# Kernel optimization log

Hardware: AMD Instinct MI355X
Metric: run time of the kernel (lower is better)

## Reference

```python
import jax, jax.numpy as jnp
import numpy as np

R, E, A, F, K = 1024, 512, 128, 32, 31  # rnn_dim, embed_dim, attn_dim, n_filters, kernel
B, T = 64, 2048


def setup_inputs() -> dict:
    key = jax.random.key(0)
    ks = jax.random.split(key, 10)
    return {
        "attention_hidden": jax.random.normal(ks[0], (B, R), jnp.float32),
        "memory": jax.random.normal(ks[1], (B, T, E), jnp.float32),
        "attention_weights_cat": jax.random.uniform(ks[2], (B, 2, T), jnp.float32),
        "mask": jax.random.randint(ks[3], (B, T), 0, 2, jnp.int32),
        "W_query": jax.random.normal(ks[4], (R, A), jnp.float32) / np.sqrt(R),
        "W_memory": jax.random.normal(ks[5], (E, A), jnp.float32) / np.sqrt(E),
        "conv_w": jax.random.normal(ks[6], (F, 2, K), jnp.float32) / np.sqrt(2 * K),  # OIH
        "W_loc": jax.random.normal(ks[7], (F, A), jnp.float32) / np.sqrt(F),
        "v_w": jax.random.normal(ks[8], (A,), jnp.float32) / np.sqrt(A),
        "v_b": jax.random.normal(ks[9], (1,), jnp.float32) * 0.0,
    }


def reference(attention_hidden, memory, attention_weights_cat, mask,
              W_query, W_memory, conv_w, W_loc, v_w, v_b):
    # processed query: (B, A)
    pq = attention_hidden @ W_query
    # processed memory: (B, T, A)
    pm = jnp.einsum('bte,ea->bta', memory, W_memory)
    # location features: conv1d over (B, 2, T) with 'same' padding, no bias
    loc = jax.lax.conv_general_dilated(
        attention_weights_cat, conv_w,
        window_strides=(1,), padding=[((K - 1) // 2, (K - 1) // 2)],
        dimension_numbers=('NCH', 'OIH', 'NCH'))  # (B, F, T)
    pl = jnp.einsum('bft,fa->bta', loc, W_loc)  # (B, T, A)
    # energies: v(tanh(pm + pq + pl)) -> (B, T)
    energies = jnp.tanh(pm + pq[:, None, :] + pl) @ v_w + v_b[0]
    alignments = energies + mask.astype(energies.dtype) * -1e25
    attention_weights = jax.nn.softmax(alignments, axis=-1)
    # NOTE: original code (faithfully) uses raw alignments, not softmax weights
    attention_output = jnp.einsum('bt,bte->be', alignments, memory)
    return attention_output, attention_weights
```

## Files before the change

kernel.cpp:

```cpp
#include <hip/hip_runtime.h>

#define Bsz 64
#define Tsz 2048
#define Esz 512
#define Asz 128
#define Rsz 1024
#define KP  576
#define TILE_M 32
#define CHUNKS (Tsz / TILE_M)

typedef __bf16 bf16;
typedef __bf16 bf16x8 __attribute__((ext_vector_type(8)));
typedef __bf16 bf16x4 __attribute__((ext_vector_type(4)));
typedef __bf16 bf16x2 __attribute__((ext_vector_type(2)));
typedef float  f32x4  __attribute__((ext_vector_type(4)));


__global__ __launch_bounds__(256) void prep_kernel(
    const float* __restrict__ Wmem, const float* __restrict__ convw,
    const float* __restrict__ Wloc, const float* __restrict__ ah,
    const float* __restrict__ Wq, bf16* __restrict__ Wext,
    float* __restrict__ pq)
{
  __shared__ f32x4 red[256];
  int blk = blockIdx.x, tid = threadIdx.x;
  if (blk < 128) {
    int a = blk;
    #pragma unroll
    for (int e = tid; e < Esz; e += 256)
      Wext[(size_t)(e >> 3)*(Asz*8) + a*8 + (e & 7)] = (bf16)Wmem[e*Asz + a];
  } else if (blk < 160) {
    int idx = (blk - 128)*256 + tid;
    int a = idx >> 6, j = idx & 63;
    float u = 0.f;
    if (j < 62) {
      int c  = (j < 31) ? 0 : 1;
      int kk = (j < 31) ? j : j - 31;
      #pragma unroll
      for (int f = 0; f < 32; ++f)
        u += convw[f*62 + c*31 + kk] * Wloc[f*Asz + a];
    }
    Wext[(size_t)(64 + (j >> 3))*(Asz*8) + a*8 + (j & 7)] = (bf16)u;
  } else {
    int b  = blk - 160;
    int cg = tid & 31;
    int kg = tid >> 5;
    const float* ahb = ah + (size_t)b*Rsz;
    f32x4 s = (f32x4){0.f,0.f,0.f,0.f};
    int r0 = kg*128;
    for (int r = r0; r < r0 + 128; ++r) {
      float av = ahb[r];
      f32x4 wq = *(const f32x4*)&Wq[r*Asz + cg*4];
      s += av * wq;
    }
    red[tid] = s;
    __syncthreads();
    if (tid < 32) {
      f32x4 tot = red[tid];
      #pragma unroll
      for (int g = 1; g < 8; ++g) tot += red[g*32 + tid];
      *(f32x4*)&pq[b*Asz + tid*4] = tot;
    }
  }
}

__device__ __forceinline__ float tanh_fast(float x) {
  float ex = __expf(2.f * x);
  return 1.f - 2.f / (ex + 1.f);
}

template<bool USE_POUT>
__global__ __launch_bounds__(256, 4) void attn_main(
    const float* __restrict__ memory, const float* __restrict__ awcat,
    const int* __restrict__ mask, const bf16* __restrict__ Wext,
    const float* __restrict__ pq, const float* __restrict__ vw,
    const float* __restrict__ vb, float* __restrict__ pout,
    float* __restrict__ outg, float* __restrict__ ws_align)
{
  __shared__ bf16  Afull[TILE_M * KP];
  __shared__ float s_pq[Asz];
  __shared__ float s_vw[Asz];
  __shared__ float s_ebuf[TILE_M];
  __shared__ float s_align[TILE_M];

  int tid = threadIdx.x;
  int b  = blockIdx.x >> 6;
  int t0 = (blockIdx.x & 63) << 5;

  int w = tid >> 6, l = tid & 63;
  int quad = l >> 4, lrow = l & 15;
  int acol0 = w*32 + lrow;
  int acol1 = acol0 + 16;
  const bf16x8* wv = (const bf16x8*)Wext;

  bf16x8 bnext0 = wv[quad*Asz + acol0];
  bf16x8 bnext1 = wv[quad*Asz + acol1];

  const f32x4* memv = (const f32x4*)(memory + (size_t)(b*Tsz + t0)*Esz);
  #pragma unroll
  for (int p = 0; p < 16; ++p) {
    int i = tid + p*256;
    int r = i >> 7, c4 = i & 127;
    f32x4 v = __builtin_nontemporal_load(memv + r*128 + c4);
    int k = c4 * 4;
    int sw = (k >> 3) ^ (r & 7);
    int base = r*KP + sw*8 + (k & 7);
    bf16x4 pk; pk[0]=(bf16)v[0]; pk[1]=(bf16)v[1]; pk[2]=(bf16)v[2]; pk[3]=(bf16)v[3];
    *(bf16x4*)&Afull[base] = pk;
  }
  const float* aw = awcat + (size_t)b*2*Tsz;
  #pragma unroll
  for (int p = 0; p < 8; ++p) {
    int i = tid + p*256;
    int r = i >> 6, j = i & 63;
    float val = 0.f;
    if (j < 62) {
      int c  = (j < 31) ? 0 : 1;
      int kk = (j < 31) ? j : j - 31;
      int t  = t0 + r + kk - 15;
      if (t >= 0 && t < Tsz) val = aw[c*Tsz + t];
    }
    int k = Esz + j;
    int sw = (k >> 3) ^ (r & 7);
    Afull[r*KP + sw*8 + (k & 7)] = (bf16)val;
  }
  if (tid < Asz) { s_pq[tid] = pq[b*Asz + tid]; s_vw[tid] = vw[tid]; }
  if (tid < TILE_M) s_ebuf[tid] = 0.f;
  __syncthreads();

  f32x4 acc[2][2];
  #pragma unroll
  for (int mt = 0; mt < 2; ++mt)
    #pragma unroll
    for (int nt = 0; nt < 2; ++nt)
      acc[mt][nt] = (f32x4){0.f, 0.f, 0.f, 0.f};

  for (int kc = 0; kc < KP/32; ++kc) {
    bf16x8 bfrag0 = bnext0, bfrag1 = bnext1;
    if (kc < KP/32 - 1) {
      int kg2 = (kc+1)*4 + quad;
      bnext0 = wv[kg2*Asz + acol0];
      bnext1 = wv[kg2*Asz + acol1];
    }
    int kg = kc*4 + quad;
    bf16x8 afrag[2];
    #pragma unroll
    for (int mt = 0; mt < 2; ++mt) {
      int row = mt*16 + lrow;
      afrag[mt] = *(const bf16x8*)&Afull[row*KP + ((kg ^ (row & 7)) << 3)];
    }
    #pragma unroll
    for (int mt = 0; mt < 2; ++mt) {
      acc[mt][0] = __builtin_amdgcn_mfma_f32_16x16x32_bf16(afrag[mt], bfrag0, acc[mt][0], 0, 0, 0);
      acc[mt][1] = __builtin_amdgcn_mfma_f32_16x16x32_bf16(afrag[mt], bfrag1, acc[mt][1], 0, 0, 0);
    }
  }

  float partial[2][4];
  #pragma unroll
  for (int mt = 0; mt < 2; ++mt)
    #pragma unroll
    for (int rg = 0; rg < 4; ++rg) partial[mt][rg] = 0.f;
  #pragma unroll
  for (int nt = 0; nt < 2; ++nt) {
    int col = w*32 + nt*16 + lrow;
    float vwc = s_vw[col], pqc = s_pq[col];
    #pragma unroll
    for (int mt = 0; mt < 2; ++mt)
      #pragma unroll
      for (int rg = 0; rg < 4; ++rg)
        partial[mt][rg] += tanh_fast(acc[mt][nt][rg] + pqc) * vwc;
  }
  #pragma unroll
  for (int off = 1; off < 16; off <<= 1)
    #pragma unroll
    for (int mt = 0; mt < 2; ++mt)
      #pragma unroll
      for (int rg = 0; rg < 4; ++rg)
        partial[mt][rg] += __shfl_xor(partial[mt][rg], off, 64);
  if (lrow == 0) {
    #pragma unroll
    for (int mt = 0; mt < 2; ++mt)
      #pragma unroll
      for (int rg = 0; rg < 4; ++rg)
        atomicAdd(&s_ebuf[mt*16 + quad*4 + rg], partial[mt][rg]);
  }
  __syncthreads();

  if (tid < TILE_M) {
    int t = t0 + tid;
    float al = s_ebuf[tid] + vb[0] + (float)mask[b*Tsz + t] * -1e25f;
    s_align[tid] = al;
    ws_align[b*Tsz + t] = al;
  }
  __syncthreads();

  int k0 = tid * 2;
  float a0 = 0.f, a1 = 0.f;
  #pragma unroll
  for (int r = 0; r < TILE_M; ++r) {
    float al = s_align[r];
    int sw = ((k0 >> 3) ^ (r & 7));
    bf16x2 m = *(const bf16x2*)&Afull[r*KP + sw*8 + (k0 & 7)];
    a0 += al * (float)m[0];
    a1 += al * (float)m[1];
  }
  if constexpr (USE_POUT) {
    float2 o; o.x = a0; o.y = a1;
    *(float2*)&pout[(size_t)blockIdx.x * Esz + k0] = o;
  } else {
    atomicAdd(&outg[b*Esz + k0],     a0);
    atomicAdd(&outg[b*Esz + k0 + 1], a1);
  }
}

template<bool REDUCE>
__global__ __launch_bounds__(256) void softmax_kernel(
    const float* __restrict__ ws_align, const float* __restrict__ pout,
    float* __restrict__ out_be, float* __restrict__ out_w)
{
  int b = blockIdx.x, tid = threadIdx.x;
  const float* row = ws_align + (size_t)b*Tsz;
  float vals[8];
  float lmax = -3.4e38f;
  #pragma unroll
  for (int i = 0; i < 8; ++i) { vals[i] = row[tid + i*256]; lmax = fmaxf(lmax, vals[i]); }
  #pragma unroll
  for (int off = 1; off < 64; off <<= 1) lmax = fmaxf(lmax, __shfl_xor(lmax, off, 64));
  __shared__ float smax[4], ssum[4];
  if ((tid & 63) == 0) smax[tid >> 6] = lmax;
  __syncthreads();
  float bmax = fmaxf(fmaxf(smax[0], smax[1]), fmaxf(smax[2], smax[3]));
  float lsum = 0.f;
  #pragma unroll
  for (int i = 0; i < 8; ++i) { vals[i] = __expf(vals[i] - bmax); lsum += vals[i]; }
  #pragma unroll
  for (int off = 1; off < 64; off <<= 1) lsum += __shfl_xor(lsum, off, 64);
  if ((tid & 63) == 0) ssum[tid >> 6] = lsum;
  __syncthreads();
  float inv = 1.f / (ssum[0] + ssum[1] + ssum[2] + ssum[3]);
  #pragma unroll
  for (int i = 0; i < 8; ++i) out_w[(size_t)b*Tsz + tid + i*256] = vals[i] * inv;

  if constexpr (REDUCE) {
    float2 s; s.x = 0.f; s.y = 0.f;
    const float2* pv = (const float2*)(pout + (size_t)b*CHUNKS*Esz) + tid;
    #pragma unroll
    for (int c = 0; c < CHUNKS; ++c) {
      float2 v = pv[(size_t)c * (Esz/2)];
      s.x += v.x; s.y += v.y;
    }
    *(float2*)&out_be[(size_t)b*Esz + tid*2] = s;
  }
}

extern "C" void kernel_launch(void* const* d_in, const int* in_sizes, int n_in,
                              void* d_out, int out_size, void* d_ws, size_t ws_size,
                              hipStream_t stream) {
  const float* ah   = (const float*)d_in[0];
  const float* mem  = (const float*)d_in[1];
  const float* awc  = (const float*)d_in[2];
  const int*   mask = (const int*)d_in[3];
  const float* Wq   = (const float*)d_in[4];
  const float* Wm   = (const float*)d_in[5];
  const float* cw   = (const float*)d_in[6];
  const float* Wl   = (const float*)d_in[7];
  const float* vw   = (const float*)d_in[8];
  const float* vb   = (const float*)d_in[9];
  float* out = (float*)d_out;

  bf16*  Wext = (bf16*)d_ws;
  float* pq   = (float*)((char*)d_ws + 147456);
  float* wsa  = (float*)((char*)d_ws + 180224);
  float* pout = (float*)((char*)d_ws + 180224 + (size_t)Bsz*Tsz*4);

  size_t need = 180224 + (size_t)Bsz*Tsz*4 + (size_t)Bsz*CHUNKS*Esz*4;

  prep_kernel<<<dim3(224), 256, 0, stream>>>(Wm, cw, Wl, ah, Wq, Wext, pq);
  if (ws_size >= need) {
    attn_main<true><<<dim3(Bsz*CHUNKS), 256, 0, stream>>>(
        mem, awc, mask, Wext, pq, vw, vb, pout, out, wsa);
    softmax_kernel<true><<<dim3(Bsz), 256, 0, stream>>>(wsa, pout, out, out + Bsz*Esz);
  } else {
    hipMemsetAsync(out, 0, Bsz*Esz*sizeof(float), stream);
    attn_main<false><<<dim3(Bsz*CHUNKS), 256, 0, stream>>>(
        mem, awc, mask, Wext, pq, vw, vb, wsa , out, wsa);
    softmax_kernel<false><<<dim3(Bsz), 256, 0, stream>>>(wsa, wsa, out, out + Bsz*Esz);
  }
}
```

Before: 435.5 us.

## Process two T-chunks per block, prefetching second memory tile into registers

Each block now handles two consecutive 32-row chunks and launches half as many blocks. The second chunk's memory tile is loaded into registers while the first chunk's MFMA and tanh work runs, then converted and written to LDS. The aim is to hide global-load latency behind compute. In exchange it holds 64 extra VGPRs of staged data and lowers launch bounds from 4 to 3 blocks per SM, which reduces occupancy.

New measurement: 499.6 us. +14.7%, slower.

```diff
diff --git a/kernel.cpp b/kernel.cpp
--- a/kernel.cpp
+++ b/kernel.cpp
@@ -69,8 +69,136 @@
   return 1.f - 2.f / (ex + 1.f);
 }
 
+__device__ __forceinline__ void stage_aw(bf16* Afull, const float* aw,
+                                         int t0p, int tid) {
+  #pragma unroll
+  for (int p = 0; p < 8; ++p) {
+    int i = tid + p*256;
+    int r = i >> 6, j = i & 63;
+    float val = 0.f;
+    if (j < 62) {
+      int c  = (j < 31) ? 0 : 1;
+      int kk = (j < 31) ? j : j - 31;
+      int t  = t0p + r + kk - 15;
+      if (t >= 0 && t < Tsz) val = aw[c*Tsz + t];
+    }
+    int k = Esz + j;
+    int sw = (k >> 3) ^ (r & 7);
+    Afull[r*KP + sw*8 + (k & 7)] = (bf16)val;
+  }
+}
+
+__device__ __forceinline__ void write_tile(bf16* Afull, const f32x4* st, int tid) {
+  #pragma unroll
+  for (int p = 0; p < 16; ++p) {
+    int i = tid + p*256;
+    int r = i >> 7, c4 = i & 127;
+    int k = c4 * 4;
+    int sw = (k >> 3) ^ (r & 7);
+    bf16x4 pk;
+    pk[0] = (bf16)st[p][0]; pk[1] = (bf16)st[p][1];
+    pk[2] = (bf16)st[p][2]; pk[3] = (bf16)st[p][3];
+    *(bf16x4*)&Afull[r*KP + sw*8 + (k & 7)] = pk;
+  }
+}
+
 template<bool USE_POUT>
-__global__ __launch_bounds__(256, 4) void attn_main(
+__device__ __forceinline__ void compute_chunk(
+    const bf16* Afull, const float* s_pq, const float* s_vw,
+    float* s_ebuf, float* s_align, const bf16x8* wv,
+    const int* __restrict__ mask, const float* __restrict__ vb,
+    float* __restrict__ pout, float* __restrict__ outg,
+    float* __restrict__ ws_align, int b, int t0p, int cid, int tid)
+{
+  int w = tid >> 6, l = tid & 63;
+  int quad = l >> 4, lrow = l & 15;
+  int acol0 = w*32 + lrow, acol1 = acol0 + 16;
+
+  f32x4 acc[2][2] = {};
+  bf16x8 bnext0 = wv[quad*Asz + acol0];
+  bf16x8 bnext1 = wv[quad*Asz + acol1];
+
+  for (int kc = 0; kc < KP/32; ++kc) {
+    bf16x8 bfrag0 = bnext0, bfrag1 = bnext1;
+    if (kc < KP/32 - 1) {
+      int kg2 = (kc+1)*4 + quad;
+      bnext0 = wv[kg2*Asz + acol0];
+      bnext1 = wv[kg2*Asz + acol1];
+    }
+    int kg = kc*4 + quad;
+    bf16x8 afrag[2];
+    #pragma unroll
+    for (int mt = 0; mt < 2; ++mt) {
+      int row = mt*16 + lrow;
+      afrag[mt] = *(const bf16x8*)&Afull[row*KP + ((kg ^ (row & 7)) << 3)];
+    }
+    #pragma unroll
+    for (int mt = 0; mt < 2; ++mt) {
+      acc[mt][0] = __builtin_amdgcn_mfma_f32_16x16x32_bf16(afrag[mt], bfrag0, acc[mt][0], 0, 0, 0);
+      acc[mt][1] = __builtin_amdgcn_mfma_f32_16x16x32_bf16(afrag[mt], bfrag1, acc[mt][1], 0, 0, 0);
+    }
+  }
+
+  float partial[2][4];
+  #pragma unroll
+  for (int mt = 0; mt < 2; ++mt)
+    #pragma unroll
+    for (int rg = 0; rg < 4; ++rg) partial[mt][rg] = 0.f;
+  #pragma unroll
+  for (int nt = 0; nt < 2; ++nt) {
+    int col = w*32 + nt*16 + lrow;
+    float vwc = s_vw[col], pqc = s_pq[col];
+    #pragma unroll
+    for (int mt = 0; mt < 2; ++mt)
+      #pragma unroll
+      for (int rg = 0; rg < 4; ++rg)
+        partial[mt][rg] += tanh_fast(acc[mt][nt][rg] + pqc) * vwc;
+  }
+  #pragma unroll
+  for (int off = 1; off < 16; off <<= 1)
+    #pragma unroll
+    for (int mt = 0; mt < 2; ++mt)
+      #pragma unroll
+      for (int rg = 0; rg < 4; ++rg)
+        partial[mt][rg] += __shfl_xor(partial[mt][rg], off, 64);
+  if (lrow == 0) {
+    #pragma unroll
+    for (int mt = 0; mt < 2; ++mt)
+      #pragma unroll
+      for (int rg = 0; rg < 4; ++rg)
+        atomicAdd(&s_ebuf[mt*16 + quad*4 + rg], partial[mt][rg]);
+  }
+  __syncthreads();
+
+  if (tid < TILE_M) {
+    int t = t0p + tid;
+    float al = s_ebuf[tid] + vb[0] + (float)mask[b*Tsz + t] * -1e25f;
+    s_align[tid] = al;
+    ws_align[b*Tsz + t] = al;
+  }
+  __syncthreads();
+
+  int k0 = tid * 2;
+  float a0 = 0.f, a1 = 0.f;
+  #pragma unroll
+  for (int r = 0; r < TILE_M; ++r) {
+    float al = s_align[r];
+    int sw = ((k0 >> 3) ^ (r & 7));
+    bf16x2 m = *(const bf16x2*)&Afull[r*KP + sw*8 + (k0 & 7)];
+    a0 += al * (float)m[0];
+    a1 += al * (float)m[1];
+  }
+  if constexpr (USE_POUT) {
+    float2 o; o.x = a0; o.y = a1;
+    *(float2*)&pout[(size_t)cid * Esz + k0] = o;
+  } else {
+    atomicAdd(&outg[b*Esz + k0],     a0);
+    atomicAdd(&outg[b*Esz + k0 + 1], a1);
+  }
+}
+
+template<bool USE_POUT>
+__global__ __launch_bounds__(256, 3) void attn_main(
     const float* __restrict__ memory, const float* __restrict__ awcat,
     const int* __restrict__ mask, const bf16* __restrict__ Wext,
     const float* __restrict__ pq, const float* __restrict__ vw,
@@ -84,134 +212,44 @@
   __shared__ float s_align[TILE_M];
 
   int tid = threadIdx.x;
-  int b  = blockIdx.x >> 6;
-  int t0 = (blockIdx.x & 63) << 5;
-
-  int w = tid >> 6, l = tid & 63;
-  int quad = l >> 4, lrow = l & 15;
-  int acol0 = w*32 + lrow;
-  int acol1 = acol0 + 16;
+  int bp = blockIdx.x;
+  int b  = bp >> 5;
+  int t0 = (bp & 31) << 6;
+
   const bf16x8* wv = (const bf16x8*)Wext;
-
-  bf16x8 bnext0 = wv[quad*Asz + acol0];
-  bf16x8 bnext1 = wv[quad*Asz + acol1];
-
-  const f32x4* memv = (const f32x4*)(memory + (size_t)(b*Tsz + t0)*Esz);
+  const float*  aw = awcat + (size_t)b*2*Tsz;
+  const f32x4*  memv = (const f32x4*)(memory + (size_t)(b*Tsz + t0)*Esz);
+
+  f32x4 st[16];
   #pragma unroll
   for (int p = 0; p < 16; ++p) {
     int i = tid + p*256;
-    int r = i >> 7, c4 = i & 127;
-    f32x4 v = __builtin_nontemporal_load(memv + r*128 + c4);
-    int k = c4 * 4;
-    int sw = (k >> 3) ^ (r & 7);
-    int base = r*KP + sw*8 + (k & 7);
-    bf16x4 pk; pk[0]=(bf16)v[0]; pk[1]=(bf16)v[1]; pk[2]=(bf16)v[2]; pk[3]=(bf16)v[3];
-    *(bf16x4*)&Afull[base] = pk;
-  }
-  const float* aw = awcat + (size_t)b*2*Tsz;
-  #pragma unroll
-  for (int p = 0; p < 8; ++p) {
-    int i = tid + p*256;
-    int r = i >> 6, j = i & 63;
-    float val = 0.f;
-    if (j < 62) {
-      int c  = (j < 31) ? 0 : 1;
-      int kk = (j < 31) ? j : j - 31;
-      int t  = t0 + r + kk - 15;
-      if (t >= 0 && t < Tsz) val = aw[c*Tsz + t];
-    }
-    int k = Esz + j;
-    int sw = (k >> 3) ^ (r & 7);
-    Afull[r*KP + sw*8 + (k & 7)] = (bf16)val;
-  }
+    st[p] = __builtin_nontemporal_load(memv + (i >> 7)*128 + (i & 127));
+  }
+  write_tile(Afull, st, tid);
+  stage_aw(Afull, aw, t0, tid);
   if (tid < Asz) { s_pq[tid] = pq[b*Asz + tid]; s_vw[tid] = vw[tid]; }
   if (tid < TILE_M) s_ebuf[tid] = 0.f;
   __syncthreads();
 
-  f32x4 acc[2][2];
-  #pragma unroll
-  for (int mt = 0; mt < 2; ++mt)
-    #pragma unroll
-    for (int nt = 0; nt < 2; ++nt)
-      acc[mt][nt] = (f32x4){0.f, 0.f, 0.f, 0.f};
-
-  for (int kc = 0; kc < KP/32; ++kc) {
-    bf16x8 bfrag0 = bnext0, bfrag1 = bnext1;
-    if (kc < KP/32 - 1) {
-      int kg2 = (kc+1)*4 + quad;
-      bnext0 = wv[kg2*Asz + acol0];
-      bnext1 = wv[kg2*Asz + acol1];
-    }
-    int kg = kc*4 + quad;
-    bf16x8 afrag[2];
-    #pragma unroll
-    for (int mt = 0; mt < 2; ++mt) {
-      int row = mt*16 + lrow;
-      afrag[mt] = *(const bf16x8*)&Afull[row*KP + ((kg ^ (row & 7)) << 3)];
-    }
-    #pragma unroll
-    for (int mt = 0; mt < 2; ++mt) {
-      acc[mt][0] = __builtin_amdgcn_mfma_f32_16x16x32_bf16(afrag[mt], bfrag0, acc[mt][0], 0, 0, 0);
-      acc[mt][1] = __builtin_amdgcn_mfma_f32_16x16x32_bf16(afrag[mt], bfrag1, acc[mt][1], 0, 0, 0);
-    }
-  }
-
-  float partial[2][4];
-  #pragma unroll
-  for (int mt = 0; mt < 2; ++mt)
-    #pragma unroll
-    for (int rg = 0; rg < 4; ++rg) partial[mt][rg] = 0.f;
-  #pragma unroll
-  for (int nt = 0; nt < 2; ++nt) {
-    int col = w*32 + nt*16 + lrow;
-    float vwc = s_vw[col], pqc = s_pq[col];
-    #pragma unroll
-    for (int mt = 0; mt < 2; ++mt)
-      #pragma unroll
-      for (int rg = 0; rg < 4; ++rg)
-        partial[mt][rg] += tanh_fast(acc[mt][nt][rg] + pqc) * vwc;
-  }
-  #pragma unroll
-  for (int off = 1; off < 16; off <<= 1)
-    #pragma unroll
-    for (int mt = 0; mt < 2; ++mt)
-      #pragma unroll
-      for (int rg = 0; rg < 4; ++rg)
-        partial[mt][rg] += __shfl_xor(partial[mt][rg], off, 64);
-  if (lrow == 0) {
-    #pragma unroll
-    for (int mt = 0; mt < 2; ++mt)
-      #pragma unroll
-      for (int rg = 0; rg < 4; ++rg)
-        atomicAdd(&s_ebuf[mt*16 + quad*4 + rg], partial[mt][rg]);
-  }
-  __syncthreads();
-
-  if (tid < TILE_M) {
-    int t = t0 + tid;
-    float al = s_ebuf[tid] + vb[0] + (float)mask[b*Tsz + t] * -1e25f;
-    s_align[tid] = al;
-    ws_align[b*Tsz + t] = al;
-  }
-  __syncthreads();
-
-  int k0 = tid * 2;
-  float a0 = 0.f, a1 = 0.f;
-  #pragma unroll
-  for (int r = 0; r < TILE_M; ++r) {
-    float al = s_align[r];
-    int sw = ((k0 >> 3) ^ (r & 7));
-    bf16x2 m = *(const bf16x2*)&Afull[r*KP + sw*8 + (k0 & 7)];
-    a0 += al * (float)m[0];
-    a1 += al * (float)m[1];
-  }
-  if constexpr (USE_POUT) {
-    float2 o; o.x = a0; o.y = a1;
-    *(float2*)&pout[(size_t)blockIdx.x * Esz + k0] = o;
-  } else {
-    atomicAdd(&outg[b*Esz + k0],     a0);
-    atomicAdd(&outg[b*Esz + k0 + 1], a1);
-  }
+  const f32x4* memv1 = memv + 32*(Esz/4);
+  #pragma unroll
+  for (int p = 0; p < 16; ++p) {
+    int i = tid + p*256;
+    st[p] = __builtin_nontemporal_load(memv1 + (i >> 7)*128 + (i & 127));
+  }
+
+  compute_chunk<USE_POUT>(Afull, s_pq, s_vw, s_ebuf, s_align, wv, mask, vb,
+                          pout, outg, ws_align, b, t0, bp << 1, tid);
+  __syncthreads();
+
+  write_tile(Afull, st, tid);
+  stage_aw(Afull, aw, t0 + 32, tid);
+  if (tid < TILE_M) s_ebuf[tid] = 0.f;
+  __syncthreads();
+
+  compute_chunk<USE_POUT>(Afull, s_pq, s_vw, s_ebuf, s_align, wv, mask, vb,
+                          pout, outg, ws_align, b, t0 + 32, (bp << 1) | 1, tid);
 }
 
 template<bool REDUCE>
@@ -278,12 +316,12 @@
 
   prep_kernel<<<dim3(224), 256, 0, stream>>>(Wm, cw, Wl, ah, Wq, Wext, pq);
   if (ws_size >= need) {
-    attn_main<true><<<dim3(Bsz*CHUNKS), 256, 0, stream>>>(
+    attn_main<true><<<dim3(Bsz*CHUNKS/2), 256, 0, stream>>>(
         mem, awc, mask, Wext, pq, vw, vb, pout, out, wsa);
     softmax_kernel<true><<<dim3(Bsz), 256, 0, stream>>>(wsa, pout, out, out + Bsz*Esz);
   } else {
     hipMemsetAsync(out, 0, Bsz*Esz*sizeof(float), stream);
-    attn_main<false><<<dim3(Bsz*CHUNKS), 256, 0, stream>>>(
+    attn_main<false><<<dim3(Bsz*CHUNKS/2), 256, 0, stream>>>(
         mem, awc, mask, Wext, pq, vw, vb, wsa , out, wsa);
     softmax_kernel<false><<<dim3(Bsz), 256, 0, stream>>>(wsa, wsa, out, out + Bsz*Esz);
   }
```
